# Performance work log

Measured on AMD Instinct MI355X. Metric: run time of the kernel, lower is better.

The kernel has to match this reference:

```python
import jax, jax.numpy as jnp
import numpy as np

B, S, D = 128, 512, 1024          # batch, ctx seqlen, model dim
GEN_V, INP_V, OUT_V = 50000, 30000, 50257  # gen vocab, input vocab, output vocab


def setup_inputs() -> dict:
    key = jax.random.key(0)
    ks = jax.random.split(key, 7)
    x = jax.random.normal(ks[0], (B, D), jnp.float32)
    alphas = jax.random.uniform(ks[1], (B, S), jnp.float32)
    alphas = alphas / alphas.sum(-1, keepdims=True)  # normalized attention probs
    ctx_inp = jax.random.randint(ks[2], (B, S), 0, INP_V)
    gen_to_out = jax.random.randint(ks[3], (GEN_V,), 0, OUT_V)
    inp_to_out = jax.random.randint(ks[4], (INP_V,), 0, OUT_V)
    W_gate = jax.random.normal(ks[5], (D, 1), jnp.float32) * 0.02
    b_gate = jnp.zeros((1,), jnp.float32)
    W_gen = jax.random.normal(ks[6], (D, GEN_V), jnp.float32) * 0.02
    b_gen = jnp.zeros((GEN_V,), jnp.float32)
    return {"x": x, "alphas": alphas, "W_gate": W_gate, "b_gate": b_gate,
            "W_gen": W_gen, "b_gen": b_gen, "ctx_inp": ctx_inp,
            "gen_to_out": gen_to_out, "inp_to_out": inp_to_out}


def reference(x, alphas, W_gate, b_gate, W_gen, b_gen, ctx_inp, gen_to_out, inp_to_out):
    # gate: probability of generating vs pointing  [B,1]
    interp = jax.nn.sigmoid(x @ W_gate + b_gate)
    # generation distribution over gen vocab       [B,GEN_V]
    gen_probs = jax.nn.softmax(x @ W_gen + b_gen, axis=-1)
    # scatter_add gen probs into output vocab (same index map for all rows)
    out_gen = jax.ops.segment_sum(gen_probs.T, gen_to_out, num_segments=OUT_V).T  # [B,OUT_V]
    # scatter_add pointer probs into output vocab (per-row indices)
    ctx_out = inp_to_out[ctx_inp]  # [B,S]
    rows = jnp.arange(x.shape[0])[:, None]
    out_ptr = jnp.zeros((x.shape[0], OUT_V), x.dtype).at[rows, ctx_out].add(alphas)
    # interpolated mixture
    return interp * out_gen + (1.0 - interp) * out_ptr
```

## Files before the change

### kernel.cpp

```cpp
#include <hip/hip_runtime.h>
#include <hip/hip_bf16.h>
#include <cstdint>
#include <cstddef>

#define B_ 128
#define D_ 1024
#define GEN_V_ 50000
#define OUT_V_ 50257
#define S_ 512

#define NTILE 128
#define NBLK 391
#define BK 64
#define LD 72
#define CAP 8

typedef __attribute__((ext_vector_type(8))) short bf16x8;
typedef __attribute__((ext_vector_type(8))) unsigned short u16x8;
typedef __attribute__((ext_vector_type(4))) float f32x4;

__device__ __forceinline__ unsigned short f2bf(float f) {
  unsigned u = __float_as_uint(f);
  u += 0x7fffu + ((u >> 16) & 1u);
  return (unsigned short)(u >> 16);
}

__global__ __launch_bounds__(512, 4) void gemm_kernel(
    const float* __restrict__ x, const float* __restrict__ W,
    const float* __restrict__ bgen, float* __restrict__ elog,
    float* __restrict__ rowpart) {
  __shared__ unsigned short sA[B_][LD];
  __shared__ unsigned short sB[NTILE][LD];
  __shared__ float srow[B_];
  int tid = threadIdx.x;
  int lane = tid & 63;
  int wv = tid >> 6;
  int wm = wv & 1;
  int wn = wv >> 1;
  int nbase = blockIdx.x * NTILE;
  int l15 = lane & 15;
  int quad = lane >> 4;
  int koff0 = quad * 8;

  f32x4 acc[4][2];
#pragma unroll
  for (int i = 0; i < 4; i++)
#pragma unroll
    for (int j = 0; j < 2; j++) acc[i][j] = (f32x4){0.f, 0.f, 0.f, 0.f};

  int bn = tid & 127;
  int kc = tid >> 7;
  bool colv = (nbase + bn) < GEN_V_;
  const float* Wcol = W + (size_t)kc * 16 * GEN_V_ + nbase + bn;

  const float4* xg = (const float4*)x;

  for (int k0 = 0; k0 < D_; k0 += BK) {
    int kb4 = k0 >> 2;
#pragma unroll
    for (int i = 0; i < 4; i++) {
      int q = tid + i * 512;
      int m = q >> 4, c4 = q & 15;
      float4 v = xg[(size_t)m * (D_ / 4) + kb4 + c4];
      ushort4 h;
      h.x = f2bf(v.x); h.y = f2bf(v.y); h.z = f2bf(v.z); h.w = f2bf(v.w);
      *(ushort4*)&sA[m][c4 * 4] = h;
    }
    {
      const float* Wp = Wcol + (size_t)k0 * GEN_V_;
      u16x8 h0, h1;
#pragma unroll
      for (int j = 0; j < 8; j++) {
        float w = colv ? Wp[(size_t)j * GEN_V_] : 0.f;
        h0[j] = f2bf(w);
      }
#pragma unroll
      for (int j = 0; j < 8; j++) {
        float w = colv ? Wp[(size_t)(j + 8) * GEN_V_] : 0.f;
        h1[j] = f2bf(w);
      }
      *(u16x8*)&sB[bn][kc * 16] = h0;
      *(u16x8*)&sB[bn][kc * 16 + 8] = h1;
    }
    __syncthreads();
#pragma unroll
    for (int ks = 0; ks < BK; ks += 32) {
      int koff = ks + koff0;
      bf16x8 bfr[2];
      bfr[0] = *(const bf16x8*)&sB[wn * 32 + l15][koff];
      bfr[1] = *(const bf16x8*)&sB[wn * 32 + 16 + l15][koff];
      bf16x8 af[4];
#pragma unroll
      for (int mt = 0; mt < 4; mt++)
        af[mt] = *(const bf16x8*)&sA[wm * 64 + mt * 16 + l15][koff];
#pragma unroll
      for (int mt = 0; mt < 4; mt++) {
        acc[mt][0] = __builtin_amdgcn_mfma_f32_16x16x32_bf16(af[mt], bfr[0], acc[mt][0], 0, 0, 0);
        acc[mt][1] = __builtin_amdgcn_mfma_f32_16x16x32_bf16(af[mt], bfr[1], acc[mt][1], 0, 0, 0);
      }
    }
    __syncthreads();
  }

  if (tid < B_) srow[tid] = 0.f;
  __syncthreads();
  int rquad = quad * 4;
#pragma unroll
  for (int nt = 0; nt < 2; nt++) {
    int cg = nbase + wn * 32 + nt * 16 + l15;
    bool cv = cg < GEN_V_;
    float bgv = cv ? bgen[cg] : 0.f;
#pragma unroll
    for (int mt = 0; mt < 4; mt++) {
      int rb = wm * 64 + mt * 16 + rquad;
#pragma unroll
      for (int r = 0; r < 4; r++) {
        float e = __expf(acc[mt][nt][r] + bgv);
        float contrib = cv ? e : 0.f;
        if (cv) elog[(size_t)(rb + r) * GEN_V_ + cg] = e;
#pragma unroll
        for (int o = 1; o < 16; o <<= 1) contrib += __shfl_xor(contrib, o);
        if (l15 == 0) atomicAdd(&srow[rb + r], contrib);
      }
    }
  }
  __syncthreads();
  if (tid < B_) rowpart[(size_t)tid * NBLK + blockIdx.x] = srow[tid];
}

__global__ void build_index_kernel(const int* __restrict__ g2o, int* __restrict__ cnt,
                                   int* __restrict__ vlist, int* __restrict__ novf,
                                   int* __restrict__ ovf) {
  int v = blockIdx.x * 256 + threadIdx.x;
  if (v < GEN_V_) {
    int o = g2o[v];
    int slot = atomicAdd(&cnt[o], 1);
    if (slot < CAP) {
      vlist[o * CAP + slot] = v;
    } else {
      int i = atomicAdd(novf, 1);
      ovf[2 * i] = o;
      ovf[2 * i + 1] = v;
    }
  }
}

__global__ void rowsum_gate_kernel(const float* __restrict__ rowpart,
                                   const float* __restrict__ x, const float* __restrict__ Wg,
                                   const float* __restrict__ bg,
                                   float* __restrict__ interp, float* __restrict__ rowscale) {
  int b = blockIdx.x, t = threadIdx.x;
  const float* rp = rowpart + (size_t)b * NBLK;
  float s = 0.f;
  for (int i = t; i < NBLK; i += 256) s += rp[i];
  const float4* xr = (const float4*)(x + (size_t)b * D_);
  const float4* wr = (const float4*)Wg;
  float4 xv = xr[t], wv = wr[t];
  float g = xv.x * wv.x + xv.y * wv.y + xv.z * wv.z + xv.w * wv.w;
  for (int o = 32; o > 0; o >>= 1) {
    s += __shfl_down(s, o);
    g += __shfl_down(g, o);
  }
  __shared__ float reds[4], redg[4];
  int lane = t & 63, w = t >> 6;
  if (lane == 0) { reds[w] = s; redg[w] = g; }
  __syncthreads();
  if (t == 0) {
    float tot = redg[0] + redg[1] + redg[2] + redg[3] + bg[0];
    float itp = 1.f / (1.f + __expf(-tot));
    float sum = reds[0] + reds[1] + reds[2] + reds[3];
    interp[b] = itp;
    rowscale[b] = itp / sum;
  }
}

#define GATHER_NB (128 * 197)
__global__ void gather_gen_kernel(const float* __restrict__ elog, const int* __restrict__ cnt,
                                  const int* __restrict__ vlist,
                                  const float* __restrict__ rowscale, float* __restrict__ out) {
  int id = blockIdx.x;
  int b = (id & 7) * 16 + ((id >> 3) & 15);
  int o = (id >> 7) * 256 + threadIdx.x;
  if (o < OUT_V_) {
    int c = cnt[o];
    if (c > CAP) c = CAP;
    const float* lrow = elog + (size_t)b * GEN_V_;
    const int* vl = vlist + (size_t)o * CAP;
    float s = 0.f;
    for (int j = 0; j < c; j++) s += lrow[vl[j]];
    out[(size_t)b * OUT_V_ + o] = s * rowscale[b];
  }
}

__global__ void ovf_kernel(const int* __restrict__ novf, const int* __restrict__ ovf,
                           const float* __restrict__ elog, const float* __restrict__ rowscale,
                           float* __restrict__ out) {
  int n = novf[0];
  if (n == 0) return;
  int total = n * B_;
  for (int i = blockIdx.x * 256 + threadIdx.x; i < total; i += gridDim.x * 256) {
    int e = i >> 7;
    int b = i & 127;
    int o = ovf[2 * e];
    int v = ovf[2 * e + 1];
    atomicAdd(&out[(size_t)b * OUT_V_ + o], rowscale[b] * elog[(size_t)b * GEN_V_ + v]);
  }
}

__global__ void scatter_ptr_kernel(const float* __restrict__ alphas, const int* __restrict__ ctx,
                                   const int* __restrict__ i2o, const float* __restrict__ interp,
                                   float* __restrict__ out) {
  int b = blockIdx.x, s = threadIdx.x;
  float w = 1.f - interp[b];
  int o = i2o[ctx[b * S_ + s]];
  atomicAdd(&out[(size_t)b * OUT_V_ + o], w * alphas[b * S_ + s]);
}

extern "C" void kernel_launch(void* const* d_in, const int* in_sizes, int n_in,
                              void* d_out, int out_size, void* d_ws, size_t ws_size,
                              hipStream_t stream) {
  const float* x      = (const float*)d_in[0];
  const float* alphas = (const float*)d_in[1];
  const float* Wg     = (const float*)d_in[2];
  const float* bg     = (const float*)d_in[3];
  const float* Wgen   = (const float*)d_in[4];
  const float* bgen   = (const float*)d_in[5];
  const int*   ctx    = (const int*)d_in[6];
  const int*   g2o    = (const int*)d_in[7];
  const int*   i2o    = (const int*)d_in[8];
  float* out = (float*)d_out;

  float* elog      = (float*)d_ws;
  float* interp    = elog + (size_t)B_ * GEN_V_;
  float* rowscale  = interp + B_;
  float* rowpart   = rowscale + B_;
  int*   cnt       = (int*)(rowpart + (size_t)B_ * NBLK);
  int*   novf      = cnt + OUT_V_;
  int*   vlist     = novf + 1;
  int*   ovf       = vlist + (size_t)OUT_V_ * CAP;

  hipMemsetAsync(cnt, 0, (OUT_V_ + 1) * sizeof(int), stream);

  build_index_kernel<<<(GEN_V_ + 255) / 256, 256, 0, stream>>>(g2o, cnt, vlist, novf, ovf);
  gemm_kernel<<<NBLK, 512, 0, stream>>>(x, Wgen, bgen, elog, rowpart);
  rowsum_gate_kernel<<<B_, 256, 0, stream>>>(rowpart, x, Wg, bg, interp, rowscale);
  gather_gen_kernel<<<GATHER_NB, 256, 0, stream>>>(elog, cnt, vlist, rowscale, out);
  ovf_kernel<<<64, 256, 0, stream>>>(novf, ovf, elog, rowscale, out);
  scatter_ptr_kernel<<<B_, S_, 0, stream>>>(alphas, ctx, i2o, interp, out);
}
```

Measured before the change: 397.7 us.

## Load GEMM operands directly from global into MFMA registers, dropping LDS staging

The GEMM kernel no longer stages x and W tiles through shared memory with barriers. Each wave now loads its own A and B fragments straight from global memory, converts them to bf16 in registers and issues the MFMAs. This removes the LDS writes, the LDS reads and two __syncthreads per K step. In exchange, x is re-read by each wave that needs it and W is fetched with strided, uncoalesced per-lane loads, with columns past the end clamped to a valid index.

```diff
diff --git a/kernel.cpp b/kernel.cpp
--- a/kernel.cpp
+++ b/kernel.cpp
@@ -12,7 +12,7 @@
 #define NTILE 128
 #define NBLK 391
 #define BK 64
-#define LD 72
+#define NSTEP (D_ / BK)
 #define CAP 8
 
 typedef __attribute__((ext_vector_type(8))) short bf16x8;
@@ -25,12 +25,17 @@
   return (unsigned short)(u >> 16);
 }
 
+__device__ __forceinline__ bf16x8 pack8(float4 lo, float4 hi) {
+  u16x8 h;
+  h[0] = f2bf(lo.x); h[1] = f2bf(lo.y); h[2] = f2bf(lo.z); h[3] = f2bf(lo.w);
+  h[4] = f2bf(hi.x); h[5] = f2bf(hi.y); h[6] = f2bf(hi.z); h[7] = f2bf(hi.w);
+  return (bf16x8)h;
+}
+
 __global__ __launch_bounds__(512, 4) void gemm_kernel(
     const float* __restrict__ x, const float* __restrict__ W,
     const float* __restrict__ bgen, float* __restrict__ elog,
     float* __restrict__ rowpart) {
-  __shared__ unsigned short sA[B_][LD];
-  __shared__ unsigned short sB[NTILE][LD];
   __shared__ float srow[B_];
   int tid = threadIdx.x;
   int lane = tid & 63;
@@ -48,58 +53,53 @@
 #pragma unroll
     for (int j = 0; j < 2; j++) acc[i][j] = (f32x4){0.f, 0.f, 0.f, 0.f};
 
-  int bn = tid & 127;
-  int kc = tid >> 7;
-  bool colv = (nbase + bn) < GEN_V_;
-  const float* Wcol = W + (size_t)kc * 16 * GEN_V_ + nbase + bn;
-
-  const float4* xg = (const float4*)x;
-
-  for (int k0 = 0; k0 < D_; k0 += BK) {
-    int kb4 = k0 >> 2;
-#pragma unroll
-    for (int i = 0; i < 4; i++) {
-      int q = tid + i * 512;
-      int m = q >> 4, c4 = q & 15;
-      float4 v = xg[(size_t)m * (D_ / 4) + kb4 + c4];
-      ushort4 h;
-      h.x = f2bf(v.x); h.y = f2bf(v.y); h.z = f2bf(v.z); h.w = f2bf(v.w);
-      *(ushort4*)&sA[m][c4 * 4] = h;
+  int n0 = nbase + wn * 32 + l15;
+  int n1 = n0 + 16;
+  unsigned n0c = (unsigned)((n0 < GEN_V_) ? n0 : (GEN_V_ - 1));
+  unsigned n1c = (unsigned)((n1 < GEN_V_) ? n1 : (GEN_V_ - 1));
+  unsigned offs0[8], offs1[8];
+#pragma unroll
+  for (int j = 0; j < 8; j++) {
+    offs0[j] = (unsigned)((koff0 + j) * GEN_V_) + n0c;
+    offs1[j] = (unsigned)((koff0 + j) * GEN_V_) + n1c;
+  }
+  const float* xp0 = x + (size_t)(wm * 64 + 0 * 16 + l15) * D_ + koff0;
+  const float* xp1 = x + (size_t)(wm * 64 + 1 * 16 + l15) * D_ + koff0;
+  const float* xp2 = x + (size_t)(wm * 64 + 2 * 16 + l15) * D_ + koff0;
+  const float* xp3 = x + (size_t)(wm * 64 + 3 * 16 + l15) * D_ + koff0;
+
+  const float* Wk = W;
+  for (int t = 0; t < NSTEP; ++t) {
+    int k0 = t * BK;
+#pragma unroll
+    for (int ks = 0; ks < 2; ks++) {
+      const float* Wh = Wk + (size_t)(ks * 32) * GEN_V_;
+      int ka = k0 + ks * 32;
+      float b0[8], b1[8];
+#pragma unroll
+      for (int j = 0; j < 8; j++) { b0[j] = Wh[offs0[j]]; b1[j] = Wh[offs1[j]]; }
+      float4 a0l = *(const float4*)(xp0 + ka), a0h = *(const float4*)(xp0 + ka + 4);
+      float4 a1l = *(const float4*)(xp1 + ka), a1h = *(const float4*)(xp1 + ka + 4);
+      float4 a2l = *(const float4*)(xp2 + ka), a2h = *(const float4*)(xp2 + ka + 4);
+      float4 a3l = *(const float4*)(xp3 + ka), a3h = *(const float4*)(xp3 + ka + 4);
+      u16x8 hb0, hb1;
+#pragma unroll
+      for (int j = 0; j < 8; j++) { hb0[j] = f2bf(b0[j]); hb1[j] = f2bf(b1[j]); }
+      bf16x8 bfr0 = (bf16x8)hb0, bfr1 = (bf16x8)hb1;
+      bf16x8 af0 = pack8(a0l, a0h);
+      bf16x8 af1 = pack8(a1l, a1h);
+      bf16x8 af2 = pack8(a2l, a2h);
+      bf16x8 af3 = pack8(a3l, a3h);
+      acc[0][0] = __builtin_amdgcn_mfma_f32_16x16x32_bf16(af0, bfr0, acc[0][0], 0, 0, 0);
+      acc[0][1] = __builtin_amdgcn_mfma_f32_16x16x32_bf16(af0, bfr1, acc[0][1], 0, 0, 0);
+      acc[1][0] = __builtin_amdgcn_mfma_f32_16x16x32_bf16(af1, bfr0, acc[1][0], 0, 0, 0);
+      acc[1][1] = __builtin_amdgcn_mfma_f32_16x16x32_bf16(af1, bfr1, acc[1][1], 0, 0, 0);
+      acc[2][0] = __builtin_amdgcn_mfma_f32_16x16x32_bf16(af2, bfr0, acc[2][0], 0, 0, 0);
+      acc[2][1] = __builtin_amdgcn_mfma_f32_16x16x32_bf16(af2, bfr1, acc[2][1], 0, 0, 0);
+      acc[3][0] = __builtin_amdgcn_mfma_f32_16x16x32_bf16(af3, bfr0, acc[3][0], 0, 0, 0);
+      acc[3][1] = __builtin_amdgcn_mfma_f32_16x16x32_bf16(af3, bfr1, acc[3][1], 0, 0, 0);
     }
-    {
-      const float* Wp = Wcol + (size_t)k0 * GEN_V_;
-      u16x8 h0, h1;
-#pragma unroll
-      for (int j = 0; j < 8; j++) {
-        float w = colv ? Wp[(size_t)j * GEN_V_] : 0.f;
-        h0[j] = f2bf(w);
-      }
-#pragma unroll
-      for (int j = 0; j < 8; j++) {
-        float w = colv ? Wp[(size_t)(j + 8) * GEN_V_] : 0.f;
-        h1[j] = f2bf(w);
-      }
-      *(u16x8*)&sB[bn][kc * 16] = h0;
-      *(u16x8*)&sB[bn][kc * 16 + 8] = h1;
-    }
-    __syncthreads();
-#pragma unroll
-    for (int ks = 0; ks < BK; ks += 32) {
-      int koff = ks + koff0;
-      bf16x8 bfr[2];
-      bfr[0] = *(const bf16x8*)&sB[wn * 32 + l15][koff];
-      bfr[1] = *(const bf16x8*)&sB[wn * 32 + 16 + l15][koff];
-      bf16x8 af[4];
-#pragma unroll
-      for (int mt = 0; mt < 4; mt++)
-        af[mt] = *(const bf16x8*)&sA[wm * 64 + mt * 16 + l15][koff];
-#pragma unroll
-      for (int mt = 0; mt < 4; mt++) {
-        acc[mt][0] = __builtin_amdgcn_mfma_f32_16x16x32_bf16(af[mt], bfr[0], acc[mt][0], 0, 0, 0);
-        acc[mt][1] = __builtin_amdgcn_mfma_f32_16x16x32_bf16(af[mt], bfr[1], acc[mt][1], 0, 0, 0);
-      }
-    }
-    __syncthreads();
+    Wk += (size_t)BK * GEN_V_;
   }
 
   if (tid < B_) srow[tid] = 0.f;
```

After: 552.2 us. +38.9%, slower.

## Pre-convert W and x to bf16 K-major staging, drop LDS tiling in GEMM

Applied to the files above, without the earlier changes.

Adds two prep kernels that convert x and W_gen to bf16 on every call. W is stored transposed per 128-column block, so each column's K values are contiguous. The GEMM then loads MFMA fragments straight from global memory with no shared-memory staging and no __syncthreads, aiming to cut the in-loop conversion and barrier overhead. In exchange it adds a full extra pass over W, and the prep kernel's writes are scattered 2-byte stores with a 2KB stride, which are poorly coalesced.

```diff
diff --git a/kernel.cpp b/kernel.cpp
--- a/kernel.cpp
+++ b/kernel.cpp
@@ -11,12 +11,12 @@
 
 #define NTILE 128
 #define NBLK 391
-#define BK 64
-#define LD 72
+#define NPAD (NBLK * 128)
 #define CAP 8
 
+#define WSTAGE_BLK_U16 (128 * 1024)
+
 typedef __attribute__((ext_vector_type(8))) short bf16x8;
-typedef __attribute__((ext_vector_type(8))) unsigned short u16x8;
 typedef __attribute__((ext_vector_type(4))) float f32x4;
 
 __device__ __forceinline__ unsigned short f2bf(float f) {
@@ -25,12 +25,41 @@
   return (unsigned short)(u >> 16);
 }
 
+__global__ void prep_x_kernel(const float* __restrict__ x, unsigned short* __restrict__ xs) {
+  int i4 = blockIdx.x * 256 + threadIdx.x;
+  float4 v = ((const float4*)x)[i4];
+  ushort4 h;
+  h.x = f2bf(v.x); h.y = f2bf(v.y); h.z = f2bf(v.z); h.w = f2bf(v.w);
+  ((ushort4*)xs)[i4] = h;
+}
+
+__global__ void prep_w_kernel(const float* __restrict__ W, unsigned short* __restrict__ ws) {
+  int g = blockIdx.x;
+  int s = blockIdx.y;
+  int tid = threadIdx.x;
+  for (int c = 0; c < 7; ++c) {
+    int width = 6256 - c * 1024; if (width > 1024) width = 1024;
+    int n4 = s * 6256 + c * 1024 + tid * 4;
+    bool act = (tid * 4 < width);
+    if (!act) continue;
+    for (int k = 0; k < 32; ++k) {
+      int kabs = g * 32 + k;
+      float4 v = make_float4(0.f, 0.f, 0.f, 0.f);
+      if (n4 < GEN_V_) v = *(const float4*)(W + (size_t)kabs * GEN_V_ + n4);
+#pragma unroll
+      for (int e = 0; e < 4; ++e) {
+        int n = n4 + e;
+        float f = (e == 0) ? v.x : (e == 1) ? v.y : (e == 2) ? v.z : v.w;
+        ws[(size_t)(n >> 7) * WSTAGE_BLK_U16 + (size_t)(n & 127) * 1024 + kabs] = f2bf(f);
+      }
+    }
+  }
+}
+
 __global__ __launch_bounds__(512, 4) void gemm_kernel(
-    const float* __restrict__ x, const float* __restrict__ W,
+    const unsigned short* __restrict__ xs, const unsigned short* __restrict__ ws,
     const float* __restrict__ bgen, float* __restrict__ elog,
     float* __restrict__ rowpart) {
-  __shared__ unsigned short sA[B_][LD];
-  __shared__ unsigned short sB[NTILE][LD];
   __shared__ float srow[B_];
   int tid = threadIdx.x;
   int lane = tid & 63;
@@ -48,58 +77,35 @@
 #pragma unroll
     for (int j = 0; j < 2; j++) acc[i][j] = (f32x4){0.f, 0.f, 0.f, 0.f};
 
-  int bn = tid & 127;
-  int kc = tid >> 7;
-  bool colv = (nbase + bn) < GEN_V_;
-  const float* Wcol = W + (size_t)kc * 16 * GEN_V_ + nbase + bn;
-
-  const float4* xg = (const float4*)x;
-
-  for (int k0 = 0; k0 < D_; k0 += BK) {
-    int kb4 = k0 >> 2;
-#pragma unroll
-    for (int i = 0; i < 4; i++) {
-      int q = tid + i * 512;
-      int m = q >> 4, c4 = q & 15;
-      float4 v = xg[(size_t)m * (D_ / 4) + kb4 + c4];
-      ushort4 h;
-      h.x = f2bf(v.x); h.y = f2bf(v.y); h.z = f2bf(v.z); h.w = f2bf(v.w);
-      *(ushort4*)&sA[m][c4 * 4] = h;
-    }
-    {
-      const float* Wp = Wcol + (size_t)k0 * GEN_V_;
-      u16x8 h0, h1;
-#pragma unroll
-      for (int j = 0; j < 8; j++) {
-        float w = colv ? Wp[(size_t)j * GEN_V_] : 0.f;
-        h0[j] = f2bf(w);
-      }
-#pragma unroll
-      for (int j = 0; j < 8; j++) {
-        float w = colv ? Wp[(size_t)(j + 8) * GEN_V_] : 0.f;
-        h1[j] = f2bf(w);
-      }
-      *(u16x8*)&sB[bn][kc * 16] = h0;
-      *(u16x8*)&sB[bn][kc * 16 + 8] = h1;
-    }
-    __syncthreads();
-#pragma unroll
-    for (int ks = 0; ks < BK; ks += 32) {
-      int koff = ks + koff0;
-      bf16x8 bfr[2];
-      bfr[0] = *(const bf16x8*)&sB[wn * 32 + l15][koff];
-      bfr[1] = *(const bf16x8*)&sB[wn * 32 + 16 + l15][koff];
-      bf16x8 af[4];
-#pragma unroll
-      for (int mt = 0; mt < 4; mt++)
-        af[mt] = *(const bf16x8*)&sA[wm * 64 + mt * 16 + l15][koff];
-#pragma unroll
-      for (int mt = 0; mt < 4; mt++) {
-        acc[mt][0] = __builtin_amdgcn_mfma_f32_16x16x32_bf16(af[mt], bfr[0], acc[mt][0], 0, 0, 0);
-        acc[mt][1] = __builtin_amdgcn_mfma_f32_16x16x32_bf16(af[mt], bfr[1], acc[mt][1], 0, 0, 0);
-      }
-    }
-    __syncthreads();
+  int nin0 = wn * 32 + l15;
+  const unsigned short* bp0 = ws + (size_t)blockIdx.x * WSTAGE_BLK_U16 + (size_t)nin0 * 1024 + koff0;
+  const unsigned short* bp1 = bp0 + 16 * 1024;
+  const unsigned short* ap0 = xs + (size_t)(wm * 64 + 0 * 16 + l15) * 1024 + koff0;
+  const unsigned short* ap1 = xs + (size_t)(wm * 64 + 1 * 16 + l15) * 1024 + koff0;
+  const unsigned short* ap2 = xs + (size_t)(wm * 64 + 2 * 16 + l15) * 1024 + koff0;
+  const unsigned short* ap3 = xs + (size_t)(wm * 64 + 3 * 16 + l15) * 1024 + koff0;
+
+  for (int t = 0; t < 4; ++t) {
+#pragma unroll
+    for (int h = 0; h < 8; ++h) {
+      int ko = h * 32;
+      bf16x8 b0 = *(const bf16x8*)(bp0 + ko);
+      bf16x8 b1 = *(const bf16x8*)(bp1 + ko);
+      bf16x8 a0 = *(const bf16x8*)(ap0 + ko);
+      bf16x8 a1 = *(const bf16x8*)(ap1 + ko);
+      bf16x8 a2 = *(const bf16x8*)(ap2 + ko);
+      bf16x8 a3 = *(const bf16x8*)(ap3 + ko);
+      acc[0][0] = __builtin_amdgcn_mfma_f32_16x16x32_bf16(a0, b0, acc[0][0], 0, 0, 0);
+      acc[0][1] = __builtin_amdgcn_mfma_f32_16x16x32_bf16(a0, b1, acc[0][1], 0, 0, 0);
+      acc[1][0] = __builtin_amdgcn_mfma_f32_16x16x32_bf16(a1, b0, acc[1][0], 0, 0, 0);
+      acc[1][1] = __builtin_amdgcn_mfma_f32_16x16x32_bf16(a1, b1, acc[1][1], 0, 0, 0);
+      acc[2][0] = __builtin_amdgcn_mfma_f32_16x16x32_bf16(a2, b0, acc[2][0], 0, 0, 0);
+      acc[2][1] = __builtin_amdgcn_mfma_f32_16x16x32_bf16(a2, b1, acc[2][1], 0, 0, 0);
+      acc[3][0] = __builtin_amdgcn_mfma_f32_16x16x32_bf16(a3, b0, acc[3][0], 0, 0, 0);
+      acc[3][1] = __builtin_amdgcn_mfma_f32_16x16x32_bf16(a3, b1, acc[3][1], 0, 0, 0);
+    }
+    bp0 += 256; bp1 += 256;
+    ap0 += 256; ap1 += 256; ap2 += 256; ap3 += 256;
   }
 
   if (tid < B_) srow[tid] = 0.f;
@@ -230,7 +236,9 @@
   const int*   i2o    = (const int*)d_in[8];
   float* out = (float*)d_out;
 
-  float* elog      = (float*)d_ws;
+  unsigned short* Wstage = (unsigned short*)d_ws;
+  unsigned short* xstage = Wstage + (size_t)NBLK * WSTAGE_BLK_U16;
+  float* elog      = (float*)(xstage + (size_t)B_ * D_);
   float* interp    = elog + (size_t)B_ * GEN_V_;
   float* rowscale  = interp + B_;
   float* rowpart   = rowscale + B_;
@@ -241,8 +249,10 @@
 
   hipMemsetAsync(cnt, 0, (OUT_V_ + 1) * sizeof(int), stream);
 
+  prep_x_kernel<<<128, 256, 0, stream>>>(x, xstage);
+  prep_w_kernel<<<dim3(32, 8), 256, 0, stream>>>(Wgen, Wstage);
   build_index_kernel<<<(GEN_V_ + 255) / 256, 256, 0, stream>>>(g2o, cnt, vlist, novf, ovf);
-  gemm_kernel<<<NBLK, 512, 0, stream>>>(x, Wgen, bgen, elog, rowpart);
+  gemm_kernel<<<NBLK, 512, 0, stream>>>(xstage, Wstage, bgen, elog, rowpart);
   rowsum_gate_kernel<<<B_, 256, 0, stream>>>(rowpart, x, Wg, bg, interp, rowscale);
   gather_gen_kernel<<<GATHER_NB, 256, 0, stream>>>(elog, cnt, vlist, rowscale, out);
   ovf_kernel<<<64, 256, 0, stream>>>(novf, ovf, elog, rowscale, out);
```

After: 1.394 ms. +250.7%, slower.
